# Performance work log

Measured on AMD Instinct MI355X. Metric: run time of the kernel, lower is better.

Reference implementation:

```python
import jax, jax.numpy as jnp
import numpy as np
from jax import lax

EPS = 1e-5

def conv2d(x, w, pad, dil):
    # x: NCHW, w: OIHW
    return lax.conv_general_dilated(
        x, w, window_strides=(1, 1), padding=[(pad, pad), (pad, pad)],
        rhs_dilation=(dil, dil), dimension_numbers=("NCHW", "OIHW", "NCHW"))

def batchnorm(x, gamma, beta):
    # training-mode BN: batch statistics over (N, H, W), biased variance
    m = x.mean(axis=(0, 2, 3), keepdims=True)
    v = x.var(axis=(0, 2, 3), keepdims=True)
    xh = (x - m) * lax.rsqrt(v + EPS)
    return gamma[None, :, None, None] * xh + beta[None, :, None, None]

def maxpool2(x):
    return lax.reduce_window(x, -jnp.inf, lax.max, (1, 1, 2, 2), (1, 1, 2, 2), "VALID")

def mhsa(x, wq, bq, wk, bk, wv, bv, rel_h, rel_w, heads=1):
    B, C, H, W = x.shape
    N = H * W
    d = C // heads
    q = (conv2d(x, wq, 0, 1) + bq[None, :, None, None]).reshape(B, heads, d, N)
    k = (conv2d(x, wk, 0, 1) + bk[None, :, None, None]).reshape(B, heads, d, N)
    v = (conv2d(x, wv, 0, 1) + bv[None, :, None, None]).reshape(B, heads, d, N)
    # content-content: q^T k -> [B, h, N, N]
    cc = jnp.einsum("bhdn,bhdm->bhnm", q, k)
    # content-position: (rel_h + rel_w) reshaped to [h, d, N], transposed, times q
    pos = (rel_h + rel_w).reshape(heads, d, N)  # broadcast-sum [1,h,d,1,H]+[1,h,d,W,1]
    cp = jnp.einsum("hnd,bhdm->bhnm", jnp.swapaxes(pos, 1, 2), q)
    attn = jax.nn.softmax(cc + cp, axis=-1)
    # out = v @ attn^T
    out = jnp.einsum("bhdn,bhmn->bhdm", v, attn)
    return out.reshape(B, C, H, W)


def setup_inputs() -> dict:
    key = jax.random.key(0)
    ks = jax.random.split(key, 16)
    B, in_ch, out_ch, S = 4, 128, 256, 64
    c4 = out_ch // 4  # 64 = MHSA channel dim
    w_scale = 0.05
    inp = {
        "x": jax.random.normal(ks[0], (B, in_ch, 2 * S, 2 * S), jnp.float32),
        "dc_w1": jax.random.normal(ks[1], (out_ch, in_ch, 3, 3), jnp.float32) * w_scale,
        "dc_b1": jnp.zeros((out_ch,), jnp.float32),
        "dc_g1": jnp.ones((out_ch,), jnp.float32),
        "dc_be1": jnp.zeros((out_ch,), jnp.float32),
        "dc_w2": jax.random.normal(ks[2], (out_ch, out_ch, 3, 3), jnp.float32) * w_scale,
        "dc_b2": jnp.zeros((out_ch,), jnp.float32),
        "dc_g2": jnp.ones((out_ch,), jnp.float32),
        "dc_be2": jnp.zeros((out_ch,), jnp.float32),
        "aspp1_w": jax.random.normal(ks[3], (c4, out_ch, 1, 1), jnp.float32) * w_scale,
        "aspp1_g": jnp.ones((c4,), jnp.float32),
        "aspp1_b": jnp.zeros((c4,), jnp.float32),
        "aspp2_w": jax.random.normal(ks[4], (c4, out_ch, 3, 3), jnp.float32) * w_scale,
        "aspp2_g": jnp.ones((c4,), jnp.float32),
        "aspp2_b": jnp.zeros((c4,), jnp.float32),
        "aspp3_w": jax.random.normal(ks[5], (c4, out_ch, 3, 3), jnp.float32) * w_scale,
        "aspp3_g": jnp.ones((c4,), jnp.float32),
        "aspp3_b": jnp.zeros((c4,), jnp.float32),
        "aspp4_w": jax.random.normal(ks[6], (c4, out_ch, 3, 3), jnp.float32) * w_scale,
        "aspp4_g": jnp.ones((c4,), jnp.float32),
        "aspp4_b": jnp.zeros((c4,), jnp.float32),
        "wq": jax.random.normal(ks[7], (c4, c4, 1, 1), jnp.float32) * w_scale,
        "bq": jnp.zeros((c4,), jnp.float32),
        "wk": jax.random.normal(ks[8], (c4, c4, 1, 1), jnp.float32) * w_scale,
        "bk": jnp.zeros((c4,), jnp.float32),
        "wv": jax.random.normal(ks[9], (c4, c4, 1, 1), jnp.float32) * w_scale,
        "bv": jnp.zeros((c4,), jnp.float32),
        "rel_h": jax.random.normal(ks[10], (1, 1, c4, 1, S), jnp.float32),
        "rel_w": jax.random.normal(ks[11], (1, 1, c4, S, 1), jnp.float32),
    }
    return inp


def reference(x, dc_w1, dc_b1, dc_g1, dc_be1, dc_w2, dc_b2, dc_g2, dc_be2,
              aspp1_w, aspp1_g, aspp1_b, aspp2_w, aspp2_g, aspp2_b,
              aspp3_w, aspp3_g, aspp3_b, aspp4_w, aspp4_g, aspp4_b,
              wq, bq, wk, bk, wv, bv, rel_h, rel_w):
    dilations = (1, 3, 6, 9)
    # mpconv: MaxPool2d(2) -> double_conv
    h = maxpool2(x)
    h = jax.nn.relu(batchnorm(conv2d(h, dc_w1, 1, 1) + dc_b1[None, :, None, None], dc_g1, dc_be1))
    h = jax.nn.relu(batchnorm(conv2d(h, dc_w2, 1, 1) + dc_b2[None, :, None, None], dc_g2, dc_be2))

    aspp = [(aspp1_w, aspp1_g, aspp1_b), (aspp2_w, aspp2_g, aspp2_b),
            (aspp3_w, aspp3_g, aspp3_b), (aspp4_w, aspp4_g, aspp4_b)]
    outs = []
    for (w, g, b), dil in zip(aspp, dilations):
        pad = 0 if dil == 1 else dil
        branch = jax.nn.relu(batchnorm(conv2d(h, w, pad, dil), g, b))
        outs.append(mhsa(branch, wq, bq, wk, bk, wv, bv, rel_h, rel_w))
    return jnp.concatenate(outs, axis=1)
```

## Files before the change

kernel.cpp:

```cpp
#include <hip/hip_runtime.h>
#include <math.h>

constexpr int Bn = 4;
constexpr int S  = 64;
constexpr int N  = 4096;

#define DEV static __device__ __forceinline__

typedef __attribute__((ext_vector_type(8))) short bf16x8;
typedef __attribute__((ext_vector_type(4))) float f32x4;

DEV unsigned short bfc(float x) {
  unsigned u = __float_as_uint(x);
  unsigned r = (u + 0x7FFFu + ((u >> 16) & 1u)) >> 16;
  return (unsigned short)r;
}

DEV void fma4(float4& a, float s, const float4 u) {
  a.x = fmaf(s, u.x, a.x); a.y = fmaf(s, u.y, a.y);
  a.z = fmaf(s, u.z, a.z); a.w = fmaf(s, u.w, a.w);
}

DEV void gload_lds16(const unsigned short* g, unsigned short* l) {
  __builtin_amdgcn_global_load_lds(
      (const __attribute__((address_space(1))) void*)g,
      (__attribute__((address_space(3))) void*)l, 16, 0, 0);
}

DEV unsigned cvtpk_bf16(float lo, float hi) {
  unsigned r;
  asm("v_cvt_pk_bf16_f32 %0, %1, %2" : "=v"(r) : "v"(lo), "v"(hi));
  return r;
}
DEV void pswap32(unsigned& a, unsigned& b) {
  asm("v_permlane32_swap_b32 %0, %1" : "+v"(a), "+v"(b));
}
DEV void pswap16(unsigned& a, unsigned& b) {
  asm("v_permlane16_swap_b32 %0, %1" : "+v"(a), "+v"(b));
}

__global__ __launch_bounds__(256) void wtr_kernel(const float* __restrict__ src,
                                                  unsigned short* __restrict__ dst,
                                                  int Cout, int Cin, int T) {
  int i = blockIdx.x * 256 + threadIdx.x;
  int ci = i % Cin;
  int r  = i / Cin;
  int t  = r / Cout;
  int co = r - t * Cout;
  dst[i] = bfc(src[((size_t)co * Cin + ci) * T + t]);
}

__global__ __launch_bounds__(256) void pool_kernel(const float* __restrict__ x,
                                                   unsigned short* __restrict__ Pp1) {
  int i = blockIdx.x * 256 + threadIdx.x;
  int xg = i & 15, y = (i >> 4) & 63, c = (i >> 10) & 127, b = i >> 17;
  const float* s = x + (((size_t)(b * 128 + c) * 128) + 2 * y) * 128 + 8 * xg;
  float4 u0 = *(const float4*)(s), u1 = *(const float4*)(s + 4);
  float4 u2 = *(const float4*)(s + 128), u3 = *(const float4*)(s + 132);
  float m0 = fmaxf(fmaxf(u0.x, u0.y), fmaxf(u2.x, u2.y));
  float m1 = fmaxf(fmaxf(u0.z, u0.w), fmaxf(u2.z, u2.w));
  float m2 = fmaxf(fmaxf(u1.x, u1.y), fmaxf(u3.x, u3.y));
  float m3 = fmaxf(fmaxf(u1.z, u1.w), fmaxf(u3.z, u3.w));
  unsigned short* d = Pp1 + (((size_t)b * 66 + y + 1) * 66 + xg * 4 + 1) * 128 + c;
  d[0] = bfc(m0); d[128] = bfc(m1); d[256] = bfc(m2); d[384] = bfc(m3);
}

template <int CTOT>
__global__ __launch_bounds__(256) void dcconv_kernel(
    const unsigned short* __restrict__ in, const unsigned short* __restrict__ wt,
    float* __restrict__ out) {
  const int Wp = 66, CSEG = CTOT / 2;
  const int w = threadIdx.x >> 6, lane = threadIdx.x & 63;
  const int ln = lane & 15, quad = lane >> 4;
  const int b = blockIdx.z >> 1, h = blockIdx.z & 1, co0 = blockIdx.y * 64;
  const int n0 = blockIdx.x * 128 + w * 32;
  const unsigned short* inb = in + (size_t)b * Wp * Wp * CTOT + h * CSEG;
  const unsigned short* wth = wt + h * CSEG;
  float* outh = out + (size_t)h * 4 * 256 * N;
  size_t pix[2];
#pragma unroll
  for (int j = 0; j < 2; j++) {
    int n = n0 + j * 16 + ln;
    int y = n >> 6, x = n & 63;
    pix[j] = ((size_t)y * Wp + x) * CTOT;
  }
  f32x4 acc[4][2];
#pragma unroll
  for (int i = 0; i < 4; i++)
#pragma unroll
    for (int j = 0; j < 2; j++) acc[i][j] = (f32x4)(0.f);
#pragma unroll
  for (int ky = 0; ky < 3; ky++)
#pragma unroll
    for (int kx = 0; kx < 3; kx++) {
      const size_t toff = ((size_t)ky * Wp + kx) * CTOT;
      const unsigned short* wtap = wth + (size_t)(ky * 3 + kx) * 256 * CTOT;
      for (int kc = 0; kc < CSEG / 32; kc++) {
        const int ko = kc * 32 + quad * 8;
        bf16x8 a[4], bb[2];
#pragma unroll
        for (int i = 0; i < 4; i++)
          a[i] = *(const bf16x8*)(wtap + (size_t)(co0 + i * 16 + ln) * CTOT + ko);
#pragma unroll
        for (int j = 0; j < 2; j++)
          bb[j] = *(const bf16x8*)(inb + pix[j] + toff + ko);
#pragma unroll
        for (int i = 0; i < 4; i++)
#pragma unroll
          for (int j = 0; j < 2; j++)
            acc[i][j] = __builtin_amdgcn_mfma_f32_16x16x32_bf16(a[i], bb[j], acc[i][j], 0, 0, 0);
      }
    }
#pragma unroll
  for (int i = 0; i < 4; i++)
#pragma unroll
    for (int j = 0; j < 2; j++)
#pragma unroll
      for (int r = 0; r < 4; r++)
        outh[((size_t)(b * 256 + co0 + i * 16 + quad * 4 + r)) * N + n0 + j * 16 + ln] =
            acc[i][j][r];
}

__global__ __launch_bounds__(256) void branch_kernel(
    const unsigned short* __restrict__ in, const unsigned short* __restrict__ wtall,
    float* __restrict__ br) {
  const int Wp = 82, halo = 9, CIN = 256;
  const int w = threadIdx.x >> 6, lane = threadIdx.x & 63;
  const int ln = lane & 15, quad = lane >> 4;
  const int bb = blockIdx.y;
  const int kbr = bb >> 2, b = bb & 3;
  const int dil = (kbr == 0) ? 1 : 3 * kbr;
  const int klo = (kbr == 0) ? 1 : 0, khi = (kbr == 0) ? 2 : 3;
  const int hd = halo - dil;
  const int cw = (w & 1) * 32, nw = (w >> 1) * 32;
  const int n0 = blockIdx.x * 64 + nw;
  const unsigned short* inb = in + (size_t)b * Wp * Wp * CIN;
  size_t pix[2];
#pragma unroll
  for (int j = 0; j < 2; j++) {
    int n = n0 + j * 16 + ln;
    int y = n >> 6, x = n & 63;
    pix[j] = ((size_t)(y + hd) * Wp + x + hd) * CIN;
  }
  f32x4 acc[2][2];
#pragma unroll
  for (int i = 0; i < 2; i++)
#pragma unroll
    for (int j = 0; j < 2; j++) acc[i][j] = (f32x4)(0.f);
  for (int ky = klo; ky < khi; ky++)
    for (int kx = klo; kx < khi; kx++) {
      const size_t toff = ((size_t)ky * Wp + kx) * dil * CIN;
      const unsigned short* wtap =
          wtall + ((size_t)kbr * 9 + ky * 3 + kx) * 64 * CIN;
      for (int kc = 0; kc < CIN / 32; kc++) {
        const int ko = kc * 32 + quad * 8;
        bf16x8 a[2], bv[2];
#pragma unroll
        for (int i = 0; i < 2; i++)
          a[i] = *(const bf16x8*)(wtap + (size_t)(cw + i * 16 + ln) * CIN + ko);
#pragma unroll
        for (int j = 0; j < 2; j++)
          bv[j] = *(const bf16x8*)(inb + pix[j] + toff + ko);
#pragma unroll
        for (int i = 0; i < 2; i++)
#pragma unroll
          for (int j = 0; j < 2; j++)
            acc[i][j] = __builtin_amdgcn_mfma_f32_16x16x32_bf16(a[i], bv[j], acc[i][j], 0, 0, 0);
      }
    }
#pragma unroll
  for (int i = 0; i < 2; i++)
#pragma unroll
    for (int j = 0; j < 2; j++)
#pragma unroll
      for (int r = 0; r < 4; r++)
        br[((size_t)bb * 64 + cw + i * 16 + quad * 4 + r) * N + n0 + j * 16 + ln] =
            acc[i][j][r];
}

__global__ __launch_bounds__(256) void bn_stats_kernel(
    const float* __restrict__ t, const float* __restrict__ gamma,
    const float* __restrict__ beta, float* __restrict__ ss, int C) {
  const int c = blockIdx.x;
  float s = 0.f, s2 = 0.f;
  for (int b = 0; b < Bn; b++) {
    const float* p = t + ((size_t)(b * C + c)) * N;
    for (int i = threadIdx.x; i < N; i += 256) {
      float v = p[i];
      s += v; s2 = fmaf(v, v, s2);
    }
  }
  for (int off = 32; off; off >>= 1) {
    s += __shfl_down(s, off, 64);
    s2 += __shfl_down(s2, off, 64);
  }
  __shared__ float rs[4], rs2[4];
  const int wid = threadIdx.x >> 6, lane = threadIdx.x & 63;
  if (lane == 0) { rs[wid] = s; rs2[wid] = s2; }
  __syncthreads();
  if (threadIdx.x == 0) {
    float S1 = rs[0] + rs[1] + rs[2] + rs[3];
    float S2 = rs2[0] + rs2[1] + rs2[2] + rs2[3];
    const float cnt = (float)(Bn * N);
    float mean = S1 / cnt;
    float var = S2 / cnt - mean * mean;
    float sc = gamma[c] * rsqrtf(var + 1e-5f);
    ss[2 * c] = sc;
    ss[2 * c + 1] = beta[c] - mean * sc;
  }
}

__global__ __launch_bounds__(256) void bn_stats2_kernel(
    const float* __restrict__ ta, const float* __restrict__ tb,
    const float* __restrict__ gamma, const float* __restrict__ beta,
    float* __restrict__ ss, int C) {
  const int c = blockIdx.x;
  float s = 0.f, s2 = 0.f;
  for (int b = 0; b < Bn; b++) {
    const size_t base = ((size_t)(b * C + c)) * N;
    for (int i = threadIdx.x; i < N; i += 256) {
      float v = ta[base + i] + tb[base + i];
      s += v; s2 = fmaf(v, v, s2);
    }
  }
  for (int off = 32; off; off >>= 1) {
    s += __shfl_down(s, off, 64);
    s2 += __shfl_down(s2, off, 64);
  }
  __shared__ float rs[4], rs2[4];
  const int wid = threadIdx.x >> 6, lane = threadIdx.x & 63;
  if (lane == 0) { rs[wid] = s; rs2[wid] = s2; }
  __syncthreads();
  if (threadIdx.x == 0) {
    float S1 = rs[0] + rs[1] + rs[2] + rs[3];
    float S2 = rs2[0] + rs2[1] + rs2[2] + rs2[3];
    const float cnt = (float)(Bn * N);
    float mean = S1 / cnt;
    float var = S2 / cnt - mean * mean;
    float sc = gamma[c] * rsqrtf(var + 1e-5f);
    ss[2 * c] = sc;
    ss[2 * c + 1] = beta[c] - mean * sc;
  }
}

__global__ __launch_bounds__(256) void bn_norm_pad2_kernel(
    const float* __restrict__ ta, const float* __restrict__ tb,
    const float* __restrict__ ss, unsigned short* __restrict__ outp,
    int Wp, int halo) {
  int i = blockIdx.x * 256 + threadIdx.x;
  int n = i & 4095, cg = (i >> 12) & 63, b = i >> 18;
  int c0 = cg * 4;
  ushort4 pk;
  float v0, v1, v2, v3;
  {
    size_t i0 = ((size_t)(b * 256 + c0 + 0)) * N + n;
    size_t i1 = i0 + N, i2 = i1 + N, i3 = i2 + N;
    v0 = fmaxf(fmaf(ta[i0] + tb[i0], ss[2 * (c0 + 0)], ss[2 * (c0 + 0) + 1]), 0.f);
    v1 = fmaxf(fmaf(ta[i1] + tb[i1], ss[2 * (c0 + 1)], ss[2 * (c0 + 1) + 1]), 0.f);
    v2 = fmaxf(fmaf(ta[i2] + tb[i2], ss[2 * (c0 + 2)], ss[2 * (c0 + 2) + 1]), 0.f);
    v3 = fmaxf(fmaf(ta[i3] + tb[i3], ss[2 * (c0 + 3)], ss[2 * (c0 + 3) + 1]), 0.f);
  }
  pk.x = bfc(v0); pk.y = bfc(v1); pk.z = bfc(v2); pk.w = bfc(v3);
  int y = n >> 6, x = n & 63;
  *(ushort4*)(outp + (((size_t)b * Wp + y + halo) * Wp + x + halo) * 256 + c0) = pk;
}

__global__ __launch_bounds__(256) void qkv_kernel(
    const float* __restrict__ br, const float* __restrict__ sta,
    const float* __restrict__ wq, const float* __restrict__ bq,
    const float* __restrict__ wk, const float* __restrict__ bk,
    const float* __restrict__ wv, const float* __restrict__ bvb,
    unsigned short* __restrict__ qTo, unsigned short* __restrict__ kTo,
    unsigned short* __restrict__ vbo) {
  const int bb = blockIdx.z;
  const int p = blockIdx.y >> 2, dg = blockIdx.y & 3;
  const float* w  = p == 0 ? wq : (p == 1 ? wk : wv);
  const float* bi = p == 0 ? bq : (p == 1 ? bk : bvb);
  __shared__ float wl[64 * 16];
  __shared__ float ssl[128];
  const int d0b = dg * 16;
  if (threadIdx.x < 128) ssl[threadIdx.x] = sta[(bb >> 2) * 128 + threadIdx.x];
  for (int i = threadIdx.x; i < 64 * 16; i += 256)
    wl[i] = w[(size_t)(d0b + (i & 15)) * 64 + (i >> 4)];
  __syncthreads();
  const int tn = threadIdx.x & 63, td = threadIdx.x >> 6;
  const int n0 = blockIdx.x * 256 + tn * 4;
  const int d0 = d0b + td * 4;
  const float* inb = br + (size_t)bb * 64 * N;
  float4 acc[4];
#pragma unroll
  for (int j = 0; j < 4; j++) {
    float bvv = bi[d0 + j];
    acc[j] = make_float4(bvv, bvv, bvv, bvv);
  }
  for (int ci = 0; ci < 64; ci++) {
    float4 u = *(const float4*)(inb + (size_t)ci * N + n0);
    const float sc = ssl[2 * ci], of = ssl[2 * ci + 1];
    u.x = fmaxf(fmaf(u.x, sc, of), 0.f);
    u.y = fmaxf(fmaf(u.y, sc, of), 0.f);
    u.z = fmaxf(fmaf(u.z, sc, of), 0.f);
    u.w = fmaxf(fmaf(u.w, sc, of), 0.f);
    float4 wv4 = *(const float4*)(wl + ci * 16 + td * 4);
    fma4(acc[0], wv4.x, u); fma4(acc[1], wv4.y, u);
    fma4(acc[2], wv4.z, u); fma4(acc[3], wv4.w, u);
  }
  const size_t slab = (size_t)bb * N * 64;
  if (p < 2) {
    unsigned short* o = (p == 0 ? qTo : kTo) + slab;
#pragma unroll
    for (int nn = 0; nn < 4; nn++) {
      ushort4 pk;
      pk.x = bfc(((const float*)&acc[0])[nn]);
      pk.y = bfc(((const float*)&acc[1])[nn]);
      pk.z = bfc(((const float*)&acc[2])[nn]);
      pk.w = bfc(((const float*)&acc[3])[nn]);
      *(ushort4*)(o + (size_t)(n0 + nn) * 64 + d0) = pk;
    }
  } else {
    unsigned short* o = vbo + slab;
#pragma unroll
    for (int j = 0; j < 4; j++) {
      ushort4 pk;
      pk.x = bfc(acc[j].x); pk.y = bfc(acc[j].y);
      pk.z = bfc(acc[j].z); pk.w = bfc(acc[j].w);
      *(ushort4*)(o + (size_t)(d0 + j) * N + n0) = pk;
    }
  }
}

__global__ __launch_bounds__(256) void posT_kernel(
    const float* __restrict__ rel_h, const float* __restrict__ rel_w,
    unsigned short* __restrict__ posT) {
  int i = blockIdx.x * 256 + threadIdx.x;
  int n = i >> 4, dq = (i & 15) * 4;
  int h = n >> 6, wc = n & 63;
  ushort4 pk;
  pk.x = bfc(rel_w[(dq + 0) * 64 + h] + rel_h[(dq + 0) * 64 + wc]);
  pk.y = bfc(rel_w[(dq + 1) * 64 + h] + rel_h[(dq + 1) * 64 + wc]);
  pk.z = bfc(rel_w[(dq + 2) * 64 + h] + rel_h[(dq + 2) * 64 + wc]);
  pk.w = bfc(rel_w[(dq + 3) * 64 + h] + rel_h[(dq + 3) * 64 + wc]);
  *(ushort4*)(posT + (size_t)n * 64 + dq) = pk;
}

__global__ __launch_bounds__(256, 3) void flash3_kernel(
    const unsigned short* __restrict__ qT, const unsigned short* __restrict__ kT,
    const unsigned short* __restrict__ posT, const unsigned short* __restrict__ vb,
    float* __restrict__ o_part, float* __restrict__ ml) {
  const int bb = blockIdx.y, split = blockIdx.z;
  const size_t slab = (size_t)bb * N * 64;
  const unsigned short* qTs = qT + slab;
  const unsigned short* kTs = kT + slab;
  const unsigned short* vbs = vb + slab;
  const int w = threadIdx.x >> 6, lane = threadIdx.x & 63;
  const int ln = lane & 15, quad = lane >> 4;
  const int m0 = blockIdx.x * 128 + w * 32;
  __shared__ __align__(16) unsigned short As[2][4][64][32];

  const unsigned short* ssrc = (w < 2) ? kTs : qTs;
  const int rsub = lane >> 2;
  const int csw  = (lane & 3) ^ ((lane >> 3) & 3);
  const int ksub = (w & 1) * 32 + csw * 8;
  auto stage = [&](int c0, int bufi) {
#pragma unroll
    for (int j = 0; j < 4; j++)
      gload_lds16(ssrc + (size_t)(c0 + j * 16 + rsub) * 64 + ksub,
                  &As[bufi][w][j * 16][0]);
  };

  bf16x8 bq[4][2];
#pragma unroll
  for (int s = 0; s < 4; s++) {
    const unsigned short* src = (s < 2) ? qTs : posT;
#pragma unroll
    for (int mf = 0; mf < 2; mf++)
      bq[s][mf] = *(const bf16x8*)(src + (size_t)(m0 + mf * 16 + ln) * 64 +
                                   (s & 1) * 32 + quad * 8);
  }

  float m_run[2] = {-3.0e38f, -3.0e38f}, l_run[2] = {0.f, 0.f};
  f32x4 o_acc[4][2];
#pragma unroll
  for (int dt = 0; dt < 4; dt++)
#pragma unroll
    for (int mf = 0; mf < 2; mf++) o_acc[dt][mf] = (f32x4)(0.f);

  const int qsw = (quad ^ ((ln >> 1) & 3)) * 8;
  const int cbeg = split * 1024;
  stage(cbeg, 0);
  for (int t = 0; t < 16; t++) {
    const int c0 = cbeg + t * 64;
    const int buf = t & 1;
    __syncthreads();
    if (t < 15) stage(c0 + 64, buf ^ 1);
    f32x4 st[4][2];
#pragma unroll
    for (int jt = 0; jt < 4; jt++)
#pragma unroll
      for (int mf = 0; mf < 2; mf++) st[jt][mf] = (f32x4)(0.f);
    __builtin_amdgcn_s_setprio(1);
#pragma unroll
    for (int s = 0; s < 4; s++) {
#pragma unroll
      for (int jt = 0; jt < 4; jt++) {
        bf16x8 a = *(const bf16x8*)(&As[buf][s][jt * 16 + ln][qsw]);
#pragma unroll
        for (int mf = 0; mf < 2; mf++)
          st[jt][mf] = __builtin_amdgcn_mfma_f32_16x16x32_bf16(a, bq[s][mf], st[jt][mf], 0, 0, 0);
      }
    }
    __builtin_amdgcn_s_setprio(0);
    unsigned P0[2][4], P1[2][4];
#pragma unroll
    for (int mf = 0; mf < 2; mf++) {
      float mx = -3.0e38f;
#pragma unroll
      for (int jt = 0; jt < 4; jt++)
#pragma unroll
        for (int r = 0; r < 4; r++) mx = fmaxf(mx, st[jt][mf][r]);
      mx = fmaxf(mx, __shfl_xor(mx, 16, 64));
      mx = fmaxf(mx, __shfl_xor(mx, 32, 64));
      if (!__all(mx <= m_run[mf])) {
        const float m_new = fmaxf(m_run[mf], mx);
        const float alpha = __expf(m_run[mf] - m_new);
        l_run[mf] *= alpha;
#pragma unroll
        for (int dt = 0; dt < 4; dt++)
#pragma unroll
          for (int r = 0; r < 4; r++) o_acc[dt][mf][r] *= alpha;
        m_run[mf] = m_new;
      }
      const float mc = m_run[mf];
      float psum = 0.f;
#pragma unroll
      for (int jt = 0; jt < 4; jt++) {
        float e0 = __expf(st[jt][mf][0] - mc);
        float e1 = __expf(st[jt][mf][1] - mc);
        float e2 = __expf(st[jt][mf][2] - mc);
        float e3 = __expf(st[jt][mf][3] - mc);
        psum += (e0 + e1) + (e2 + e3);
        P0[mf][jt] = cvtpk_bf16(e0, e1);
        P1[mf][jt] = cvtpk_bf16(e2, e3);
      }
      psum += __shfl_xor(psum, 16, 64);
      psum += __shfl_xor(psum, 32, 64);
      l_run[mf] += psum;
    }
    __builtin_amdgcn_s_setprio(1);
#pragma unroll
    for (int tt = 0; tt < 2; tt++) {
      bf16x8 av[4];
#pragma unroll
      for (int dt = 0; dt < 4; dt++)
        av[dt] = *(const bf16x8*)(vbs + (size_t)(dt * 16 + ln) * N + c0 + tt * 32 + quad * 8);
#pragma unroll
      for (int mf = 0; mf < 2; mf++) {
        unsigned x0 = P0[mf][2 * tt], y0 = P0[mf][2 * tt + 1];
        pswap32(x0, y0); pswap16(x0, y0);
        unsigned x1 = P1[mf][2 * tt], y1 = P1[mf][2 * tt + 1];
        pswap32(x1, y1); pswap16(x1, y1);
        union { unsigned u[4]; bf16x8 v; } bp;
        bp.u[0] = x0; bp.u[1] = x1; bp.u[2] = y0; bp.u[3] = y1;
#pragma unroll
        for (int dt = 0; dt < 4; dt++)
          o_acc[dt][mf] = __builtin_amdgcn_mfma_f32_16x16x32_bf16(av[dt], bp.v, o_acc[dt][mf], 0, 0, 0);
      }
    }
    __builtin_amdgcn_s_setprio(0);
  }
  float* ob = o_part + ((size_t)(split * 16 + bb) * 64) * N;
#pragma unroll
  for (int dt = 0; dt < 4; dt++)
#pragma unroll
    for (int mf = 0; mf < 2; mf++)
#pragma unroll
      for (int r = 0; r < 4; r++) {
        int d = dt * 16 + quad * 4 + r;
        ob[(size_t)d * N + m0 + mf * 16 + ln] = o_acc[dt][mf][r];
      }
  if (quad == 0) {
#pragma unroll
    for (int mf = 0; mf < 2; mf++) {
      int m = m0 + mf * 16 + ln;
      ml[((size_t)(split * 16 + bb) * 2 + 0) * N + m] = m_run[mf];
      ml[((size_t)(split * 16 + bb) * 2 + 1) * N + m] = l_run[mf];
    }
  }
}

__global__ __launch_bounds__(256) void wcomb_kernel(const float* __restrict__ ml,
                                                    float* __restrict__ wcb) {
  int i = blockIdx.x * 256 + threadIdx.x;
  int m = i & 4095, bb = i >> 12;
  float mv[4], lv[4];
#pragma unroll
  for (int s = 0; s < 4; s++) {
    mv[s] = ml[((size_t)(s * 16 + bb) * 2 + 0) * N + m];
    lv[s] = ml[((size_t)(s * 16 + bb) * 2 + 1) * N + m];
  }
  float M = fmaxf(fmaxf(mv[0], mv[1]), fmaxf(mv[2], mv[3]));
  float wsc[4], denom = 0.f;
#pragma unroll
  for (int s = 0; s < 4; s++) {
    wsc[s] = __expf(mv[s] - M);
    denom = fmaf(wsc[s], lv[s], denom);
  }
  float inv = 1.0f / denom;
#pragma unroll
  for (int s = 0; s < 4; s++)
    wcb[(size_t)(s * 16 + bb) * N + m] = wsc[s] * inv;
}

__global__ __launch_bounds__(256) void comb_kernel(const float* __restrict__ o_part,
                                                   const float* __restrict__ wcb,
                                                   float* __restrict__ out) {
  int i = blockIdx.x * 256 + threadIdx.x;
  int m4 = i & 1023, d = (i >> 10) & 63, bb = i >> 16;
  int kbr = bb >> 2, b = bb & 3;
  float4 acc = make_float4(0.f, 0.f, 0.f, 0.f);
#pragma unroll
  for (int s = 0; s < 4; s++) {
    const float4 o = *(const float4*)(o_part + ((size_t)(s * 16 + bb) * 64 + d) * N + m4 * 4);
    const float4 wv = *(const float4*)(wcb + (size_t)(s * 16 + bb) * N + m4 * 4);
    acc.x = fmaf(o.x, wv.x, acc.x); acc.y = fmaf(o.y, wv.y, acc.y);
    acc.z = fmaf(o.z, wv.z, acc.z); acc.w = fmaf(o.w, wv.w, acc.w);
  }
  *(float4*)(out + ((size_t)(b * 256 + kbr * 64 + d)) * N + m4 * 4) = acc;
}

extern "C" void kernel_launch(void* const* d_in, const int* in_sizes, int n_in,
                              void* d_out, int out_size, void* d_ws, size_t ws_size,
                              hipStream_t stream) {
  const float* x      = (const float*)d_in[0];
  const float* dc_w1  = (const float*)d_in[1];
  const float* dc_g1  = (const float*)d_in[3];
  const float* dc_be1 = (const float*)d_in[4];
  const float* dc_w2  = (const float*)d_in[5];
  const float* dc_g2  = (const float*)d_in[7];
  const float* dc_be2 = (const float*)d_in[8];
  const float* aspp_w[4] = {(const float*)d_in[9],  (const float*)d_in[12],
                            (const float*)d_in[15], (const float*)d_in[18]};
  const float* aspp_g[4] = {(const float*)d_in[10], (const float*)d_in[13],
                            (const float*)d_in[16], (const float*)d_in[19]};
  const float* aspp_b[4] = {(const float*)d_in[11], (const float*)d_in[14],
                            (const float*)d_in[17], (const float*)d_in[20]};
  const float* wq = (const float*)d_in[21];
  const float* bq = (const float*)d_in[22];
  const float* wk = (const float*)d_in[23];
  const float* bk = (const float*)d_in[24];
  const float* wv = (const float*)d_in[25];
  const float* bv = (const float*)d_in[26];
  const float* rel_h = (const float*)d_in[27];
  const float* rel_w = (const float*)d_in[28];
  float* out = (float*)d_out;

  float* ws = (float*)d_ws;
  size_t off = 0;
  auto alloc = [&](size_t nf) { float* p = ws + off; off += nf; return p; };
  unsigned short* Pp1 = (unsigned short*)alloc((size_t)4 * 66 * 66 * 128 / 2 + 64);
  unsigned short* Pp2 = (unsigned short*)alloc((size_t)4 * 66 * 66 * 256 / 2 + 64);
  unsigned short* Pp3 = (unsigned short*)alloc((size_t)4 * 82 * 82 * 256 / 2 + 64);
  const size_t HALF = (size_t)4 * 256 * N;
  float* t1   = alloc(2 * HALF);
  float* br   = alloc((size_t)4 * 4 * 64 * N);
  float* st1  = alloc(512);
  float* st2  = alloc(512);
  float* sta  = alloc(512);
  unsigned short* qT    = (unsigned short*)alloc((size_t)16 * N * 64 / 2);
  unsigned short* kT    = (unsigned short*)alloc((size_t)16 * N * 64 / 2);
  unsigned short* vb    = (unsigned short*)alloc((size_t)16 * N * 64 / 2);
  unsigned short* posT  = (unsigned short*)alloc((size_t)N * 64 / 2);
  unsigned short* wt1   = (unsigned short*)alloc((size_t)9 * 256 * 128 / 2);
  unsigned short* wt2   = (unsigned short*)alloc((size_t)9 * 256 * 256 / 2);
  unsigned short* wtbr  = (unsigned short*)alloc((size_t)4 * 9 * 64 * 256 / 2);
  float* o_part = alloc((size_t)4 * 16 * 64 * N);
  float* mlb    = alloc((size_t)4 * 16 * 2 * N);
  float* wcb    = alloc((size_t)4 * 16 * N);

  hipMemsetAsync(Pp1, 0, (size_t)4 * 66 * 66 * 128 * 2, stream);
  hipMemsetAsync(Pp2, 0, (size_t)4 * 66 * 66 * 256 * 2, stream);
  hipMemsetAsync(Pp3, 0, (size_t)4 * 82 * 82 * 256 * 2, stream);
  hipMemsetAsync(wtbr, 0, (size_t)4 * 9 * 64 * 256 * 2, stream);

  wtr_kernel<<<(9 * 256 * 128) / 256, 256, 0, stream>>>(dc_w1, wt1, 256, 128, 9);
  wtr_kernel<<<(9 * 256 * 256) / 256, 256, 0, stream>>>(dc_w2, wt2, 256, 256, 9);
  wtr_kernel<<<(64 * 256) / 256, 256, 0, stream>>>(
      aspp_w[0], wtbr + (size_t)4 * 64 * 256, 64, 256, 1);
  for (int kbr = 1; kbr < 4; kbr++)
    wtr_kernel<<<(9 * 64 * 256) / 256, 256, 0, stream>>>(
        aspp_w[kbr], wtbr + (size_t)kbr * 9 * 64 * 256, 64, 256, 9);

  pool_kernel<<<2048, 256, 0, stream>>>(x, Pp1);

  dcconv_kernel<128><<<dim3(32, 4, 8), 256, 0, stream>>>(Pp1, wt1, t1);
  bn_stats2_kernel<<<256, 256, 0, stream>>>(t1, t1 + HALF, dc_g1, dc_be1, st1, 256);
  bn_norm_pad2_kernel<<<4096, 256, 0, stream>>>(t1, t1 + HALF, st1, Pp2, 66, 1);
  dcconv_kernel<256><<<dim3(32, 4, 8), 256, 0, stream>>>(Pp2, wt2, t1);
  bn_stats2_kernel<<<256, 256, 0, stream>>>(t1, t1 + HALF, dc_g2, dc_be2, st2, 256);
  bn_norm_pad2_kernel<<<4096, 256, 0, stream>>>(t1, t1 + HALF, st2, Pp3, 82, 9);

  branch_kernel<<<dim3(64, 16), 256, 0, stream>>>(Pp3, wtbr, br);
  for (int kbr = 0; kbr < 4; kbr++)
    bn_stats_kernel<<<64, 256, 0, stream>>>(br + (size_t)kbr * 1048576,
                                            aspp_g[kbr], aspp_b[kbr],
                                            sta + kbr * 128, 64);

  qkv_kernel<<<dim3(16, 12, 16), 256, 0, stream>>>(br, sta, wq, bq, wk, bk,
                                                   wv, bv, qT, kT, vb);
  posT_kernel<<<256, 256, 0, stream>>>(rel_h, rel_w, posT);

  flash3_kernel<<<dim3(32, 16, 4), 256, 0, stream>>>(qT, kT, posT, vb, o_part, mlb);
  wcomb_kernel<<<256, 256, 0, stream>>>(mlb, wcb);
  comb_kernel<<<4096, 256, 0, stream>>>(o_part, wcb, out);
}
```

Before: 772.0 us.

## Remap flash grid for XCD locality, hoist V loads, fuse BN stats launches

The flash attention kernel now runs on a 1D grid. Block indices are remapped so that each XCD (the low 3 bits of the block index) handles only two batch-slabs, which should keep K/Q/V reuse inside one XCD's L2. The V-fragment loads are moved ahead of the softmax so their global latency overlaps the exp and max work, and the max reduction is rebalanced into a tree. The four per-branch BN statistics launches are merged into one 256-block launch. Holding the hoisted V fragments raises register pressure, which may reduce occupancy under the 3-block launch bound.

```diff
diff --git a/kernel.cpp b/kernel.cpp
--- a/kernel.cpp
+++ b/kernel.cpp
@@ -178,13 +178,21 @@
             acc[i][j][r];
 }
 
-__global__ __launch_bounds__(256) void bn_stats_kernel(
-    const float* __restrict__ t, const float* __restrict__ gamma,
-    const float* __restrict__ beta, float* __restrict__ ss, int C) {
-  const int c = blockIdx.x;
+__global__ __launch_bounds__(256) void bn_stats_all_kernel(
+    const float* __restrict__ br,
+    const float* __restrict__ g0, const float* __restrict__ b0,
+    const float* __restrict__ g1, const float* __restrict__ b1,
+    const float* __restrict__ g2, const float* __restrict__ b2,
+    const float* __restrict__ g3, const float* __restrict__ b3,
+    float* __restrict__ sta) {
+  const int kbr = blockIdx.x >> 6, c = blockIdx.x & 63;
+  const float* gamma = kbr == 0 ? g0 : (kbr == 1 ? g1 : (kbr == 2 ? g2 : g3));
+  const float* beta  = kbr == 0 ? b0 : (kbr == 1 ? b1 : (kbr == 2 ? b2 : b3));
+  const float* t = br + (size_t)kbr * 1048576;
+  float* ss = sta + kbr * 128;
   float s = 0.f, s2 = 0.f;
   for (int b = 0; b < Bn; b++) {
-    const float* p = t + ((size_t)(b * C + c)) * N;
+    const float* p = t + ((size_t)(b * 64 + c)) * N;
     for (int i = threadIdx.x; i < N; i += 256) {
       float v = p[i];
       s += v; s2 = fmaf(v, v, s2);
@@ -346,14 +354,18 @@
     const unsigned short* __restrict__ qT, const unsigned short* __restrict__ kT,
     const unsigned short* __restrict__ posT, const unsigned short* __restrict__ vb,
     float* __restrict__ o_part, float* __restrict__ ml) {
-  const int bb = blockIdx.y, split = blockIdx.z;
+  const int lin = blockIdx.x;
+  const int xcd = lin & 7, slot = lin >> 3;
+  const int bb = xcd * 2 + (slot & 1);
+  const int rest = slot >> 1;
+  const int mtile = rest & 31, split = rest >> 5;
   const size_t slab = (size_t)bb * N * 64;
   const unsigned short* qTs = qT + slab;
   const unsigned short* kTs = kT + slab;
   const unsigned short* vbs = vb + slab;
   const int w = threadIdx.x >> 6, lane = threadIdx.x & 63;
   const int ln = lane & 15, quad = lane >> 4;
-  const int m0 = blockIdx.x * 128 + w * 32;
+  const int m0 = mtile * 128 + w * 32;
   __shared__ __align__(16) unsigned short As[2][4][64][32];
 
   const unsigned short* ssrc = (w < 2) ? kTs : qTs;
@@ -409,14 +421,21 @@
       }
     }
     __builtin_amdgcn_s_setprio(0);
+    bf16x8 av[2][4];
+#pragma unroll
+    for (int tt = 0; tt < 2; tt++)
+#pragma unroll
+      for (int dt = 0; dt < 4; dt++)
+        av[tt][dt] = *(const bf16x8*)(vbs + (size_t)(dt * 16 + ln) * N + c0 + tt * 32 + quad * 8);
     unsigned P0[2][4], P1[2][4];
 #pragma unroll
     for (int mf = 0; mf < 2; mf++) {
-      float mx = -3.0e38f;
+      float mj[4];
 #pragma unroll
       for (int jt = 0; jt < 4; jt++)
-#pragma unroll
-        for (int r = 0; r < 4; r++) mx = fmaxf(mx, st[jt][mf][r]);
+        mj[jt] = fmaxf(fmaxf(st[jt][mf][0], st[jt][mf][1]),
+                       fmaxf(st[jt][mf][2], st[jt][mf][3]));
+      float mx = fmaxf(fmaxf(mj[0], mj[1]), fmaxf(mj[2], mj[3]));
       mx = fmaxf(mx, __shfl_xor(mx, 16, 64));
       mx = fmaxf(mx, __shfl_xor(mx, 32, 64));
       if (!__all(mx <= m_run[mf])) {
@@ -448,10 +467,6 @@
     __builtin_amdgcn_s_setprio(1);
 #pragma unroll
     for (int tt = 0; tt < 2; tt++) {
-      bf16x8 av[4];
-#pragma unroll
-      for (int dt = 0; dt < 4; dt++)
-        av[dt] = *(const bf16x8*)(vbs + (size_t)(dt * 16 + ln) * N + c0 + tt * 32 + quad * 8);
 #pragma unroll
       for (int mf = 0; mf < 2; mf++) {
         unsigned x0 = P0[mf][2 * tt], y0 = P0[mf][2 * tt + 1];
@@ -462,7 +477,7 @@
         bp.u[0] = x0; bp.u[1] = x1; bp.u[2] = y0; bp.u[3] = y1;
 #pragma unroll
         for (int dt = 0; dt < 4; dt++)
-          o_acc[dt][mf] = __builtin_amdgcn_mfma_f32_16x16x32_bf16(av[dt], bp.v, o_acc[dt][mf], 0, 0, 0);
+          o_acc[dt][mf] = __builtin_amdgcn_mfma_f32_16x16x32_bf16(av[tt][dt], bp.v, o_acc[dt][mf], 0, 0, 0);
       }
     }
     __builtin_amdgcn_s_setprio(0);
@@ -599,16 +614,15 @@
   bn_norm_pad2_kernel<<<4096, 256, 0, stream>>>(t1, t1 + HALF, st2, Pp3, 82, 9);
 
   branch_kernel<<<dim3(64, 16), 256, 0, stream>>>(Pp3, wtbr, br);
-  for (int kbr = 0; kbr < 4; kbr++)
-    bn_stats_kernel<<<64, 256, 0, stream>>>(br + (size_t)kbr * 1048576,
-                                            aspp_g[kbr], aspp_b[kbr],
-                                            sta + kbr * 128, 64);
+  bn_stats_all_kernel<<<256, 256, 0, stream>>>(
+      br, aspp_g[0], aspp_b[0], aspp_g[1], aspp_b[1],
+      aspp_g[2], aspp_b[2], aspp_g[3], aspp_b[3], sta);
 
   qkv_kernel<<<dim3(16, 12, 16), 256, 0, stream>>>(br, sta, wq, bq, wk, bk,
                                                    wv, bv, qT, kT, vb);
   posT_kernel<<<256, 256, 0, stream>>>(rel_h, rel_w, posT);
 
-  flash3_kernel<<<dim3(32, 16, 4), 256, 0, stream>>>(qT, kT, posT, vb, o_part, mlb);
+  flash3_kernel<<<dim3(2048), 256, 0, stream>>>(qT, kT, posT, vb, o_part, mlb);
   wcomb_kernel<<<256, 256, 0, stream>>>(mlb, wcb);
   comb_kernel<<<4096, 256, 0, stream>>>(o_part, wcb, out);
 }
```

Result: faster. 703.7 us (-8.9%).
